# Optimization experiments

Hardware: AMD Instinct MI355X
Metric: run time of the kernel (lower is better)

The kernel has to match this reference:

```python
import jax, jax.numpy as jnp
import numpy as np

NUM_GRAPHS = 100
NODES_PER_GRAPH = 400
UND_EDGES_PER_GRAPH = 5000  # -> 10000 directed edges per graph
UNITS = 64


def setup_inputs() -> dict:
    rng = np.random.default_rng(0)
    g = np.repeat(np.arange(NUM_GRAPHS), UND_EDGES_PER_GRAPH)
    src_l = rng.integers(0, NODES_PER_GRAPH, g.shape[0])
    dst_l = rng.integers(0, NODES_PER_GRAPH, g.shape[0])
    # avoid self loops (molecular graphs have none by default)
    dst_l = np.where(dst_l == src_l, (dst_l + 1) % NODES_PER_GRAPH, dst_l)
    src = (g * NODES_PER_GRAPH + src_l).astype(np.int32)
    dst = (g * NODES_PER_GRAPH + dst_l).astype(np.int32)
    # both directions, as produced by molecular graph encoders
    edge_src = jnp.asarray(np.concatenate([src, dst]))
    edge_dst = jnp.asarray(np.concatenate([dst, src]))
    E = edge_src.shape[0]
    num_nodes = NUM_GRAPHS * NODES_PER_GRAPH
    graph_indicator = jnp.asarray(
        np.repeat(np.arange(NUM_GRAPHS), NODES_PER_GRAPH).astype(np.int32))
    key = jax.random.key(0)
    k1, k2 = jax.random.split(key)
    edge_feature = jax.random.normal(k1, (E, UNITS), dtype=jnp.float32)
    W = jax.random.normal(k2, (2 * UNITS, UNITS), dtype=jnp.float32) * 0.005
    b = jnp.zeros((UNITS,), dtype=jnp.float32)
    return {"edge_feature": edge_feature, "edge_src": edge_src,
            "edge_dst": edge_dst, "graph_indicator": graph_indicator,
            "num_nodes": num_nodes, "W": W, "b": b}


def _reverse_edge_features(edge_feature, edge_src, edge_dst, num_nodes):
    # For each edge i, sum of edge_feature[j] over all j with
    # (src_j, dst_j) == (dst_i, src_i). Node ids are disjoint across
    # subgraphs, so a global (src,dst) key match is equivalent to the
    # per-subgraph match done by the original tf.map_fn version.
    E = edge_feature.shape[0]
    key = edge_src * num_nodes + edge_dst          # fits int32 for N<=46k
    rev = edge_dst * num_nodes + edge_src
    perm = jnp.argsort(key)
    sk = key[perm]
    # group duplicate keys (multi-edges) and sum their features
    new_grp = jnp.concatenate(
        [jnp.zeros((1,), sk.dtype), (sk[1:] != sk[:-1]).astype(sk.dtype)])
    gid = jnp.cumsum(new_grp)                      # [E] group id per sorted edge
    group_sum = jax.ops.segment_sum(edge_feature[perm], gid, num_segments=E)
    pos = jnp.clip(jnp.searchsorted(sk, rev), 0, E - 1)
    match = sk[pos] == rev
    return jnp.where(match[:, None], group_sum[gid[pos]], 0.0)


def reference(edge_feature, edge_src, edge_dst, graph_indicator, num_nodes, W, b):
    # message step: aggregate incoming edge states at each node, gather back
    # to each edge's source node, subtract the reverse edge's own state
    agg = jax.ops.segment_sum(edge_feature, edge_dst, num_segments=num_nodes)
    message = agg[edge_src] - _reverse_edge_features(
        edge_feature, edge_src, edge_dst, num_nodes)
    # update step: Dense(relu) on concat([prev_state, message])
    h = jnp.concatenate([edge_feature, message], axis=1)
    return jax.nn.relu(h @ W + b)
```

## Files before the change

kernel.cpp:

```cpp
#include <hip/hip_runtime.h>
#include <cstdint>
#include <cstddef>

#define OA_LOG 21
static constexpr unsigned OA_SLOTS = 1u << OA_LOG;
static constexpr unsigned OA_MASK  = OA_SLOTS - 1;
static constexpr unsigned HASH_MUL = 2654435761u;

typedef __attribute__((ext_vector_type(8))) short short8;
typedef __attribute__((ext_vector_type(4))) float floatx4;

union U4S8 { uint4 u; short8 s; };

__device__ inline unsigned bf16rn(float x) {
    unsigned u = __float_as_uint(x);
    return (u + 0x7FFFu + ((u >> 16) & 1u)) >> 16;
}
__device__ inline unsigned pk2(float a, float b) {
    return bf16rn(a) | (bf16rn(b) << 16);
}

__global__ void wpack_kernel(const float* __restrict__ W, uint4* __restrict__ wsW) {
    const int lane = threadIdx.x;
    const int n = lane & 15, q = lane >> 4;
    for (int s = 0; s < 4; ++s)
        for (int t = 0; t < 4; ++t) {
            unsigned dw[4];
#pragma unroll
            for (int jj = 0; jj < 4; ++jj) {
                float a = W[(32 * s + 8 * q + 2 * jj) * 64 + 16 * t + n];
                float b = W[(32 * s + 8 * q + 2 * jj + 1) * 64 + 16 * t + n];
                dw[jj] = pk2(a, b);
            }
            wsW[(s * 4 + t) * 64 + lane] = make_uint4(dw[0], dw[1], dw[2], dw[3]);
        }
}

__global__ void hist_kernel(const int* __restrict__ edst, int* __restrict__ cnt, int E) {
    int e = blockIdx.x * blockDim.x + threadIdx.x;
    if (e < E) atomicAdd(&cnt[edst[e]], 1);
}

__global__ void scan_kernel(int* __restrict__ cnt, int* __restrict__ off, int NN, int E) {
    __shared__ int sd[1024];
    const int t = threadIdx.x;
    const int chunk = (NN + 1023) >> 10;
    const int lo = t * chunk, hi = min(lo + chunk, NN);
    int local = 0;
    for (int i = lo; i < hi; ++i) local += cnt[i];
    sd[t] = local;
    __syncthreads();
    for (int s = 1; s < 1024; s <<= 1) {
        int v = (t >= s) ? sd[t - s] : 0;
        __syncthreads();
        sd[t] += v;
        __syncthreads();
    }
    int run = sd[t] - local;
    for (int i = lo; i < hi; ++i) {
        int c = cnt[i];
        off[i] = run;
        cnt[i] = run;
        run += c;
    }
    if (t == 0) off[NN] = E;
}

__global__ void scatter_kernel(const int* __restrict__ edst, int* __restrict__ cursor,
                               int* __restrict__ csr, int E) {
    int e = blockIdx.x * blockDim.x + threadIdx.x;
    if (e >= E) return;
    int slot = atomicAdd(&cursor[edst[e]], 1);
    csr[slot] = e;
}

__global__ __launch_bounds__(256)
void agg_csr_kernel(const float* __restrict__ feat, const int* __restrict__ csr,
                    const int* __restrict__ off, float* __restrict__ agg, int NN) {
    const int wid = (blockIdx.x * blockDim.x + threadIdx.x) >> 6;
    const int lane = threadIdx.x & 63;
    if (wid >= NN) return;
    const int i0 = off[wid], i1 = off[wid + 1];
    float acc = 0.f;
    int i = i0;
    for (; i + 4 <= i1; i += 4) {
        int c0 = csr[i], c1 = csr[i + 1], c2 = csr[i + 2], c3 = csr[i + 3];
        float a0 = feat[((long long)c0 << 6) + lane];
        float a1 = feat[((long long)c1 << 6) + lane];
        float a2 = feat[((long long)c2 << 6) + lane];
        float a3 = feat[((long long)c3 << 6) + lane];
        acc += (a0 + a1) + (a2 + a3);
    }
    for (; i < i1; ++i) acc += feat[((long long)csr[i] << 6) + lane];
    agg[((long long)wid << 6) + lane] = acc;
}

__global__ void build_oa_kernel(const int* __restrict__ esrc,
                                const int* __restrict__ edst,
                                unsigned long long* __restrict__ tbl,
                                int E, unsigned NN) {
    int e = blockIdx.x * blockDim.x + threadIdx.x;
    if (e >= E) return;
    unsigned k = (unsigned)esrc[e] * NN + (unsigned)edst[e];
    unsigned long long mine = ((unsigned long long)(unsigned)e << 32) | (unsigned long long)k;
    unsigned s = (k * HASH_MUL) >> (32 - OA_LOG);
    const unsigned long long EMPTY = ~0ull;
    while (atomicCAS(&tbl[s], EMPTY, mine) != EMPTY)
        s = (s + 1) & OA_MASK;
}

__global__ void mark_rev_kernel(const int* __restrict__ esrc,
                                const int* __restrict__ edst,
                                const unsigned long long* __restrict__ tbl,
                                int* __restrict__ revid,
                                int E, unsigned NN) {
    int e = blockIdx.x * blockDim.x + threadIdx.x;
    if (e >= E) return;
    unsigned rk = (unsigned)edst[e] * NN + (unsigned)esrc[e];
    unsigned s = (rk * HASH_MUL) >> (32 - OA_LOG);
    int cnt = 0, idx = -1;
    while (true) {
        unsigned long long v = tbl[s];
        if ((unsigned)v == 0xFFFFFFFFu) break;
        if ((unsigned)v == rk) { ++cnt; idx = (int)(v >> 32); }
        s = (s + 1) & OA_MASK;
    }
    revid[e] = (cnt == 1) ? idx : -1;
}

__global__ __launch_bounds__(256, 2)
void fused_kernel(const float* __restrict__ feat,
                  const int* __restrict__ esrc,
                  const int* __restrict__ edst,
                  const float* __restrict__ agg,
                  const unsigned long long* __restrict__ tbl,
                  const int* __restrict__ revid,
                  const uint4* __restrict__ wsW,
                  const float* __restrict__ bias,
                  float* __restrict__ out,
                  int E, unsigned NN) {
    __shared__ unsigned lds_h[64 * 68];
    const int tid = threadIdx.x;
    const int lane = tid & 63;
    const int n = lane & 15;
    const int q = lane >> 4;
    const int g = blockIdx.x;
    const long long H = (long long)(E >> 1);
    const bool paired = (E & 63) == 0;

    short8 wf[4][4];
#pragma unroll
    for (int s = 0; s < 4; ++s)
#pragma unroll
        for (int t = 0; t < 4; ++t) {
            U4S8 cvt;
            cvt.u = wsW[(s * 4 + t) * 64 + lane];
            wf[s][t] = cvt.s;
        }
    float bv[4];
#pragma unroll
    for (int t = 0; t < 4; ++t) bv[t] = bias[16 * t + n];

    const int el = tid >> 2;
    const int p = tid & 3;
    long long e;
    if (paired) e = (long long)g * 32 + (el & 31) + (long long)(el >> 5) * H;
    else        e = (long long)g * 64 + el;

    float4 f0, f1, f2, f3, m0, m1, m2, m3;
    if (e < (long long)E) {
        const float4* fp = (const float4*)(feat + (e << 6) + 16 * p);
        f0 = fp[0]; f1 = fp[1]; f2 = fp[2]; f3 = fp[3];
        const int s_ = esrc[e], d_ = edst[e];
        const float4* ap = (const float4*)(agg + ((long long)s_ << 6) + 16 * p);
        m0 = ap[0]; m1 = ap[1]; m2 = ap[2]; m3 = ap[3];

        const int rid = revid[e];
        float4 r0, r1, r2, r3;
        if (rid >= 0) {
            const float4* rp = (const float4*)(feat + ((long long)rid << 6) + 16 * p);
            r0 = rp[0]; r1 = rp[1]; r2 = rp[2]; r3 = rp[3];
        } else {
            r0 = r1 = r2 = r3 = make_float4(0.f, 0.f, 0.f, 0.f);
            const unsigned rk = (unsigned)d_ * NN + (unsigned)s_;
            unsigned slot = (rk * HASH_MUL) >> (32 - OA_LOG);
            while (true) {
                unsigned long long v = tbl[slot];
                if ((unsigned)v == 0xFFFFFFFFu) break;
                if ((unsigned)v == rk) {
                    const float4* rp =
                        (const float4*)(feat + ((long long)(v >> 32) << 6) + 16 * p);
                    float4 a0 = rp[0], a1 = rp[1], a2 = rp[2], a3 = rp[3];
                    r0.x += a0.x; r0.y += a0.y; r0.z += a0.z; r0.w += a0.w;
                    r1.x += a1.x; r1.y += a1.y; r1.z += a1.z; r1.w += a1.w;
                    r2.x += a2.x; r2.y += a2.y; r2.z += a2.z; r2.w += a2.w;
                    r3.x += a3.x; r3.y += a3.y; r3.z += a3.z; r3.w += a3.w;
                }
                slot = (slot + 1) & OA_MASK;
            }
        }
        m0.x -= r0.x; m0.y -= r0.y; m0.z -= r0.z; m0.w -= r0.w;
        m1.x -= r1.x; m1.y -= r1.y; m1.z -= r1.z; m1.w -= r1.w;
        m2.x -= r2.x; m2.y -= r2.y; m2.z -= r2.z; m2.w -= r2.w;
        m3.x -= r3.x; m3.y -= r3.y; m3.z -= r3.z; m3.w -= r3.w;
    } else {
        f0 = f1 = f2 = f3 = make_float4(0.f, 0.f, 0.f, 0.f);
        m0 = m1 = m2 = m3 = make_float4(0.f, 0.f, 0.f, 0.f);
    }
    unsigned* row = &lds_h[el * 68];
    *(uint4*)(row + 8 * p) =
        make_uint4(pk2(f0.x, f0.y), pk2(f0.z, f0.w), pk2(f1.x, f1.y), pk2(f1.z, f1.w));
    *(uint4*)(row + 8 * p + 4) =
        make_uint4(pk2(f2.x, f2.y), pk2(f2.z, f2.w), pk2(f3.x, f3.y), pk2(f3.z, f3.w));
    *(uint4*)(row + 32 + 8 * p) =
        make_uint4(pk2(m0.x, m0.y), pk2(m0.z, m0.w), pk2(m1.x, m1.y), pk2(m1.z, m1.w));
    *(uint4*)(row + 32 + 8 * p + 4) =
        make_uint4(pk2(m2.x, m2.y), pk2(m2.z, m2.w), pk2(m3.x, m3.y), pk2(m3.z, m3.w));
    __syncthreads();

    const int w = tid >> 6;
    floatx4 acc[4];
#pragma unroll
    for (int t = 0; t < 4; ++t) acc[t] = (floatx4){0.f, 0.f, 0.f, 0.f};
#pragma unroll
    for (int s = 0; s < 4; ++s) {
        U4S8 a;
        a.u = *(const uint4*)&lds_h[(16 * w + n) * 68 + 16 * s + 4 * q];
#pragma unroll
        for (int t = 0; t < 4; ++t)
            acc[t] = __builtin_amdgcn_mfma_f32_16x16x32_bf16(a.s, wf[s][t], acc[t], 0, 0, 0);
    }

#pragma unroll
    for (int r = 0; r < 4; ++r) {
        const int rowi = 16 * w + 4 * q + r;
        long long ee;
        if (paired) ee = (long long)g * 32 + (rowi & 31) + (long long)(rowi >> 5) * H;
        else        ee = (long long)g * 64 + rowi;
        if (ee < (long long)E) {
#pragma unroll
            for (int t = 0; t < 4; ++t) {
                float v = acc[t][r] + bv[t];
                out[(ee << 6) + 16 * t + n] = v > 0.f ? v : 0.f;
            }
        }
    }
}

extern "C" void kernel_launch(void* const* d_in, const int* in_sizes, int n_in,
                              void* d_out, int out_size, void* d_ws, size_t ws_size,
                              hipStream_t stream) {
    const float* feat = (const float*)d_in[0];
    const int*   esrc = (const int*)d_in[1];
    const int*   edst = (const int*)d_in[2];
    const float* W    = (const float*)d_in[5];
    const float* bias = (const float*)d_in[6];
    float* out = (float*)d_out;

    const int E  = in_sizes[1];
    const int NN = in_sizes[3];

    char* ws = (char*)d_ws;
    size_t o = 0;
    auto alloc = [&](size_t bytes) { void* p = ws + o; o = (o + bytes + 15) & ~(size_t)15; return p; };
    float* agg   = (float*)alloc((size_t)NN * 64 * sizeof(float));
    int*   cnt   = (int*)alloc((size_t)NN * sizeof(int));
    int*   off   = (int*)alloc((size_t)(NN + 1) * sizeof(int));
    int*   csr   = (int*)alloc((size_t)E * sizeof(int));
    unsigned long long* tbl = (unsigned long long*)alloc((size_t)OA_SLOTS * 8);
    int*   revid = (int*)alloc((size_t)E * sizeof(int));
    uint4* wsW   = (uint4*)alloc((size_t)16 * 64 * sizeof(uint4));

    hipMemsetAsync(cnt, 0, (size_t)NN * sizeof(int), stream);
    hipMemsetAsync(tbl, 0xFF, (size_t)OA_SLOTS * 8, stream);

    const int eb = (E + 255) / 256;
    wpack_kernel<<<1, 64, 0, stream>>>(W, wsW);
    hist_kernel<<<eb, 256, 0, stream>>>(edst, cnt, E);
    scan_kernel<<<1, 1024, 0, stream>>>(cnt, off, NN, E);
    scatter_kernel<<<eb, 256, 0, stream>>>(edst, cnt, csr, E);
    build_oa_kernel<<<eb, 256, 0, stream>>>(esrc, edst, tbl, E, (unsigned)NN);
    mark_rev_kernel<<<eb, 256, 0, stream>>>(esrc, edst, tbl, revid, E, (unsigned)NN);
    agg_csr_kernel<<<(NN + 3) / 4, 256, 0, stream>>>(feat, csr, off, agg, NN);
    fused_kernel<<<(E + 63) / 64, 256, 0, stream>>>(
        feat, esrc, edst, agg, tbl, revid, wsW, bias, out, E, (unsigned)NN);
}
```

Measured before the change: 838.5 us.

## Replace reverse-edge hash pass with dense per-graph lookup table and fuse build kernels

Adds a direct-addressed table indexed by (node, local node within a block of 400), filled during a fused histogram and hash-build kernel. The fused kernel now looks up the reverse edge there and falls back to hash probing only for duplicates or cross-block pairs. This drops the separate build_oa and mark_rev launches and their passes over the hash table. The cost is a 64 MB memset and scattered atomics into that table. Other changes: the aggregation loop is unrolled to 8 gathers, the fused kernel's occupancy hint goes from 2 to 4 blocks, and the weight-fragment loads move after the gather phase to lower register pressure.

```diff
diff --git a/kernel.cpp b/kernel.cpp
--- a/kernel.cpp
+++ b/kernel.cpp
@@ -6,6 +6,8 @@
 static constexpr unsigned OA_SLOTS = 1u << OA_LOG;
 static constexpr unsigned OA_MASK  = OA_SLOTS - 1;
 static constexpr unsigned HASH_MUL = 2654435761u;
+static constexpr unsigned GSZ = 400;
+static constexpr unsigned DENSE_DUP = 0xFFFFFFFFu;
 
 typedef __attribute__((ext_vector_type(8))) short short8;
 typedef __attribute__((ext_vector_type(4))) float floatx4;
@@ -36,9 +38,32 @@
         }
 }
 
-__global__ void hist_kernel(const int* __restrict__ edst, int* __restrict__ cnt, int E) {
+__global__ void prep_build_kernel(const int* __restrict__ esrc,
+                                  const int* __restrict__ edst,
+                                  int* __restrict__ cnt,
+                                  unsigned long long* __restrict__ tbl,
+                                  unsigned* __restrict__ dense,
+                                  int E, unsigned NN) {
     int e = blockIdx.x * blockDim.x + threadIdx.x;
-    if (e < E) atomicAdd(&cnt[edst[e]], 1);
+    if (e >= E) return;
+    const unsigned s = (unsigned)esrc[e], d = (unsigned)edst[e];
+    atomicAdd(&cnt[d], 1);
+
+    unsigned k = s * NN + d;
+    unsigned long long mine = ((unsigned long long)(unsigned)e << 32) | (unsigned long long)k;
+    unsigned slot = (k * HASH_MUL) >> (32 - OA_LOG);
+    const unsigned long long EMPTY = ~0ull;
+    while (atomicCAS(&tbl[slot], EMPTY, mine) != EMPTY)
+        slot = (slot + 1) & OA_MASK;
+
+    if (dense) {
+        const unsigned gs = s / GSZ, gd = d / GSZ;
+        if (gs == gd) {
+            unsigned dk = s * GSZ + (d - gd * GSZ);
+            unsigned old = atomicCAS(&dense[dk], 0u, (unsigned)e + 1u);
+            if (old != 0u) atomicExch(&dense[dk], DENSE_DUP);
+        }
+    }
 }
 
 __global__ void scan_kernel(int* __restrict__ cnt, int* __restrict__ off, int NN, int E) {
@@ -72,41 +97,6 @@
     if (e >= E) return;
     int slot = atomicAdd(&cursor[edst[e]], 1);
     csr[slot] = e;
-}
-
-__global__ __launch_bounds__(256)
-void agg_csr_kernel(const float* __restrict__ feat, const int* __restrict__ csr,
-                    const int* __restrict__ off, float* __restrict__ agg, int NN) {
-    const int wid = (blockIdx.x * blockDim.x + threadIdx.x) >> 6;
-    const int lane = threadIdx.x & 63;
-    if (wid >= NN) return;
-    const int i0 = off[wid], i1 = off[wid + 1];
-    float acc = 0.f;
-    int i = i0;
-    for (; i + 4 <= i1; i += 4) {
-        int c0 = csr[i], c1 = csr[i + 1], c2 = csr[i + 2], c3 = csr[i + 3];
-        float a0 = feat[((long long)c0 << 6) + lane];
-        float a1 = feat[((long long)c1 << 6) + lane];
-        float a2 = feat[((long long)c2 << 6) + lane];
-        float a3 = feat[((long long)c3 << 6) + lane];
-        acc += (a0 + a1) + (a2 + a3);
-    }
-    for (; i < i1; ++i) acc += feat[((long long)csr[i] << 6) + lane];
-    agg[((long long)wid << 6) + lane] = acc;
-}
-
-__global__ void build_oa_kernel(const int* __restrict__ esrc,
-                                const int* __restrict__ edst,
-                                unsigned long long* __restrict__ tbl,
-                                int E, unsigned NN) {
-    int e = blockIdx.x * blockDim.x + threadIdx.x;
-    if (e >= E) return;
-    unsigned k = (unsigned)esrc[e] * NN + (unsigned)edst[e];
-    unsigned long long mine = ((unsigned long long)(unsigned)e << 32) | (unsigned long long)k;
-    unsigned s = (k * HASH_MUL) >> (32 - OA_LOG);
-    const unsigned long long EMPTY = ~0ull;
-    while (atomicCAS(&tbl[s], EMPTY, mine) != EMPTY)
-        s = (s + 1) & OA_MASK;
 }
 
 __global__ void mark_rev_kernel(const int* __restrict__ esrc,
@@ -128,13 +118,37 @@
     revid[e] = (cnt == 1) ? idx : -1;
 }
 
-__global__ __launch_bounds__(256, 2)
+__global__ __launch_bounds__(256)
+void agg_csr_kernel(const float* __restrict__ feat, const int* __restrict__ csr,
+                    const int* __restrict__ off, float* __restrict__ agg, int NN) {
+    const int wid = (blockIdx.x * blockDim.x + threadIdx.x) >> 6;
+    const int lane = threadIdx.x & 63;
+    if (wid >= NN) return;
+    const int i0 = off[wid], i1 = off[wid + 1];
+    float acc = 0.f;
+    int i = i0;
+    for (; i + 8 <= i1; i += 8) {
+        int c[8];
+#pragma unroll
+        for (int j = 0; j < 8; ++j) c[j] = csr[i + j];
+        float a[8];
+#pragma unroll
+        for (int j = 0; j < 8; ++j) a[j] = feat[((long long)c[j] << 6) + lane];
+        acc += ((a[0] + a[1]) + (a[2] + a[3])) + ((a[4] + a[5]) + (a[6] + a[7]));
+    }
+    for (; i < i1; ++i) acc += feat[((long long)csr[i] << 6) + lane];
+    agg[((long long)wid << 6) + lane] = acc;
+}
+
+__global__ __launch_bounds__(256, 4)
 void fused_kernel(const float* __restrict__ feat,
                   const int* __restrict__ esrc,
                   const int* __restrict__ edst,
                   const float* __restrict__ agg,
                   const unsigned long long* __restrict__ tbl,
+                  const unsigned* __restrict__ dense,
                   const int* __restrict__ revid,
+                  int use_dense,
                   const uint4* __restrict__ wsW,
                   const float* __restrict__ bias,
                   float* __restrict__ out,
@@ -148,19 +162,6 @@
     const long long H = (long long)(E >> 1);
     const bool paired = (E & 63) == 0;
 
-    short8 wf[4][4];
-#pragma unroll
-    for (int s = 0; s < 4; ++s)
-#pragma unroll
-        for (int t = 0; t < 4; ++t) {
-            U4S8 cvt;
-            cvt.u = wsW[(s * 4 + t) * 64 + lane];
-            wf[s][t] = cvt.s;
-        }
-    float bv[4];
-#pragma unroll
-    for (int t = 0; t < 4; ++t) bv[t] = bias[16 * t + n];
-
     const int el = tid >> 2;
     const int p = tid & 3;
     long long e;
@@ -175,13 +176,27 @@
         const float4* ap = (const float4*)(agg + ((long long)s_ << 6) + 16 * p);
         m0 = ap[0]; m1 = ap[1]; m2 = ap[2]; m3 = ap[3];
 
-        const int rid = revid[e];
+        int rid = -1;
+        bool slow = false;
+        if (use_dense) {
+            const unsigned gs = (unsigned)s_ / GSZ, gd = (unsigned)d_ / GSZ;
+            if (gs == gd) {
+                unsigned v = dense[(unsigned)d_ * GSZ + ((unsigned)s_ - gs * GSZ)];
+                if (v == 0u) {  }
+                else if (v == DENSE_DUP) slow = true;
+                else rid = (int)(v - 1u);
+            } else slow = true;
+        } else {
+            rid = revid[e];
+            if (rid < 0) slow = true;
+        }
+
         float4 r0, r1, r2, r3;
+        r0 = r1 = r2 = r3 = make_float4(0.f, 0.f, 0.f, 0.f);
         if (rid >= 0) {
             const float4* rp = (const float4*)(feat + ((long long)rid << 6) + 16 * p);
             r0 = rp[0]; r1 = rp[1]; r2 = rp[2]; r3 = rp[3];
-        } else {
-            r0 = r1 = r2 = r3 = make_float4(0.f, 0.f, 0.f, 0.f);
+        } else if (slow) {
             const unsigned rk = (unsigned)d_ * NN + (unsigned)s_;
             unsigned slot = (rk * HASH_MUL) >> (32 - OA_LOG);
             while (true) {
@@ -218,6 +233,19 @@
         make_uint4(pk2(m2.x, m2.y), pk2(m2.z, m2.w), pk2(m3.x, m3.y), pk2(m3.z, m3.w));
     __syncthreads();
 
+    short8 wf[4][4];
+#pragma unroll
+    for (int s = 0; s < 4; ++s)
+#pragma unroll
+        for (int t = 0; t < 4; ++t) {
+            U4S8 cvt;
+            cvt.u = wsW[(s * 4 + t) * 64 + lane];
+            wf[s][t] = cvt.s;
+        }
+    float bv[4];
+#pragma unroll
+    for (int t = 0; t < 4; ++t) bv[t] = bias[16 * t + n];
+
     const int w = tid >> 6;
     floatx4 acc[4];
 #pragma unroll
@@ -268,20 +296,26 @@
     int*   off   = (int*)alloc((size_t)(NN + 1) * sizeof(int));
     int*   csr   = (int*)alloc((size_t)E * sizeof(int));
     unsigned long long* tbl = (unsigned long long*)alloc((size_t)OA_SLOTS * 8);
+    uint4* wsW   = (uint4*)alloc((size_t)16 * 64 * sizeof(uint4));
     int*   revid = (int*)alloc((size_t)E * sizeof(int));
-    uint4* wsW   = (uint4*)alloc((size_t)16 * 64 * sizeof(uint4));
+    const size_t dense_elems = (size_t)NN * GSZ;
+    unsigned* dense = (unsigned*)alloc(dense_elems * sizeof(unsigned));
+    const int use_dense = (o <= ws_size) ? 1 : 0;
 
     hipMemsetAsync(cnt, 0, (size_t)NN * sizeof(int), stream);
     hipMemsetAsync(tbl, 0xFF, (size_t)OA_SLOTS * 8, stream);
+    if (use_dense)
+        hipMemsetAsync(dense, 0, dense_elems * sizeof(unsigned), stream);
 
     const int eb = (E + 255) / 256;
     wpack_kernel<<<1, 64, 0, stream>>>(W, wsW);
-    hist_kernel<<<eb, 256, 0, stream>>>(edst, cnt, E);
+    prep_build_kernel<<<eb, 256, 0, stream>>>(esrc, edst, cnt, tbl,
+                                              use_dense ? dense : nullptr, E, (unsigned)NN);
     scan_kernel<<<1, 1024, 0, stream>>>(cnt, off, NN, E);
     scatter_kernel<<<eb, 256, 0, stream>>>(edst, cnt, csr, E);
-    build_oa_kernel<<<eb, 256, 0, stream>>>(esrc, edst, tbl, E, (unsigned)NN);
-    mark_rev_kernel<<<eb, 256, 0, stream>>>(esrc, edst, tbl, revid, E, (unsigned)NN);
+    if (!use_dense)
+        mark_rev_kernel<<<eb, 256, 0, stream>>>(esrc, edst, tbl, revid, E, (unsigned)NN);
     agg_csr_kernel<<<(NN + 3) / 4, 256, 0, stream>>>(feat, csr, off, agg, NN);
     fused_kernel<<<(E + 63) / 64, 256, 0, stream>>>(
-        feat, esrc, edst, agg, tbl, revid, wsW, bias, out, E, (unsigned)NN);
-}
+        feat, esrc, edst, agg, tbl, dense, revid, use_dense, wsW, bias, out, E, (unsigned)NN);
+}
```

Result: slower. 905.2 us (+8.0%).
